# Performance work log

Hardware: AMD Instinct MI355X
Metric: run time of the kernel (lower is better)

Reference implementation:

```python
import jax, jax.numpy as jnp
import numpy as np

B, LQ, LK, E, H, F = 4, 1024, 1024, 1024, 16, 4096
DH = E // H
SCALE = 1.0 / float(np.sqrt(DH))


def _ln(x, g, b, eps=1e-5):
    m = jnp.mean(x, axis=-1, keepdims=True)
    v = jnp.mean((x - m) ** 2, axis=-1, keepdims=True)
    return (x - m) * jax.lax.rsqrt(v + eps) * g + b


def setup_inputs() -> dict:
    key = jax.random.key(0)
    ks = jax.random.split(key, 16)
    s = 0.02
    return {
        "tgt": jax.random.normal(ks[0], (B, LQ, E), jnp.float32),
        "memory": jax.random.normal(ks[1], (B, LK, E), jnp.float32),
        "ln1_g": jnp.ones((E,), jnp.float32),
        "ln1_b": jnp.zeros((E,), jnp.float32),
        "wq": jax.random.normal(ks[2], (E, E), jnp.float32) * s,
        "bq": jnp.zeros((E,), jnp.float32),
        "wk": jax.random.normal(ks[3], (E, E), jnp.float32) * s,
        "bk": jnp.zeros((E,), jnp.float32),
        "wv": jax.random.normal(ks[4], (E, E), jnp.float32) * s,
        "bv": jnp.zeros((E,), jnp.float32),
        "wo": jax.random.normal(ks[5], (E, E), jnp.float32) * s,
        "bo": jnp.zeros((E,), jnp.float32),
        "ln3_g": jnp.ones((E,), jnp.float32),
        "ln3_b": jnp.zeros((E,), jnp.float32),
        "w1": jax.random.normal(ks[6], (E, F), jnp.float32) * s,
        "b1": jnp.zeros((F,), jnp.float32),
        "w2": jax.random.normal(ks[7], (F, E), jnp.float32) * s,
        "b2": jnp.zeros((E,), jnp.float32),
    }


def reference(tgt, memory, ln1_g, ln1_b, wq, bq, wk, bk, wv, bv, wo, bo,
              ln3_g, ln3_b, w1, b1, w2, b2):
    # prenorm cross-attention (dropout=0 / eval mode)
    t2 = _ln(tgt, ln1_g, ln1_b)
    q = (t2 @ wq + bq).reshape(B, LQ, H, DH)
    k = (memory @ wk + bk).reshape(B, LK, H, DH)
    v = (memory @ wv + bv).reshape(B, LK, H, DH)
    scores = jnp.einsum('bqhd,bkhd->bhqk', q, k) * SCALE
    p = jax.nn.softmax(scores, axis=-1)          # [B,H,Lq,Lk]
    attn = jnp.mean(p, axis=1)                   # averaged over heads, like torch need_weights
    o = jnp.einsum('bhqk,bkhd->bqhd', p, v).reshape(B, LQ, E) @ wo + bo
    x = tgt + o
    # prenorm FFN
    t3 = _ln(x, ln3_g, ln3_b)
    ffn = jax.nn.relu(t3 @ w1 + b1) @ w2 + b2
    return x + ffn, attn
```

## Files before the change

kernel.cpp:

```cpp
#include <hip/hip_runtime.h>
#include <hip/hip_bf16.h>

using short8 = __attribute__((ext_vector_type(8))) short;
using f32x4  = __attribute__((ext_vector_type(4))) float;
using u16x4  = __attribute__((ext_vector_type(4))) unsigned short;

#define AS1 __attribute__((address_space(1)))
#define AS3 __attribute__((address_space(3)))

__device__ __forceinline__ unsigned short f2bf(float f) {
    __hip_bfloat16 h = __float2bfloat16(f);
    return __builtin_bit_cast(unsigned short, h);
}

__device__ __forceinline__ float exp2_hw(float x) {
    float r;
    asm("v_exp_f32 %0, %1" : "=v"(r) : "v"(x));
    return r;
}

__device__ __forceinline__ int vperm(int lk) {
    return (lk & ~31) | (((lk >> 2) & 3) * 8) | (((lk >> 4) & 1) * 4) | (lk & 3);
}

__global__ __launch_bounds__(256) void ln_to_bf16(
    const float* __restrict__ X, const float* __restrict__ gw,
    const float* __restrict__ bw, unsigned short* __restrict__ Y)
{
    const int row = blockIdx.x;
    const int tid = threadIdx.x;
    const float4 v = *(const float4*)(X + (size_t)row * 1024 + tid * 4);
    float s  = v.x + v.y + v.z + v.w;
    float s2 = v.x*v.x + v.y*v.y + v.z*v.z + v.w*v.w;
    #pragma unroll
    for (int off = 1; off < 64; off <<= 1) {
        s  += __shfl_xor(s,  off);
        s2 += __shfl_xor(s2, off);
    }
    __shared__ float rs[4], rq[4];
    if ((tid & 63) == 0) { rs[tid >> 6] = s; rq[tid >> 6] = s2; }
    __syncthreads();
    s  = rs[0] + rs[1] + rs[2] + rs[3];
    s2 = rq[0] + rq[1] + rq[2] + rq[3];
    const float mean = s * (1.f / 1024.f);
    const float var  = s2 * (1.f / 1024.f) - mean * mean;
    const float rstd = rsqrtf(var + 1e-5f);
    const float4 gv = *(const float4*)(gw + tid * 4);
    const float4 bv = *(const float4*)(bw + tid * 4);
    u16x4 o;
    o[0] = f2bf((v.x - mean) * rstd * gv.x + bv.x);
    o[1] = f2bf((v.y - mean) * rstd * gv.y + bv.y);
    o[2] = f2bf((v.z - mean) * rstd * gv.z + bv.z);
    o[3] = f2bf((v.w - mean) * rstd * gv.w + bv.w);
    *(u16x4*)(Y + (size_t)row * 1024 + tid * 4) = o;
}

__global__ __launch_bounds__(256) void prep_fused(
    const float* __restrict__ tgt, const float* __restrict__ ln1g,
    const float* __restrict__ ln1b, unsigned short* __restrict__ XA,
    const float* __restrict__ mem, unsigned short* __restrict__ M16,
    const float* __restrict__ wq, const float* __restrict__ wk,
    const float* __restrict__ wv, const float* __restrict__ wo,
    unsigned short* __restrict__ WQT, unsigned short* __restrict__ WKT,
    unsigned short* __restrict__ WVT, unsigned short* __restrict__ WOT,
    const float* __restrict__ w1, unsigned short* __restrict__ W1T,
    const float* __restrict__ w2, unsigned short* __restrict__ W2T)
{
    __shared__ float t[32][33];
    __shared__ float rs[4], rq[4];
    const int bid = blockIdx.x;
    const int tid = threadIdx.x;
    if (bid < 4096) {
        const int row = bid;
        const float4 v = *(const float4*)(tgt + (size_t)row * 1024 + tid * 4);
        float s  = v.x + v.y + v.z + v.w;
        float s2 = v.x*v.x + v.y*v.y + v.z*v.z + v.w*v.w;
        #pragma unroll
        for (int off = 1; off < 64; off <<= 1) {
            s  += __shfl_xor(s,  off);
            s2 += __shfl_xor(s2, off);
        }
        if ((tid & 63) == 0) { rs[tid >> 6] = s; rq[tid >> 6] = s2; }
        __syncthreads();
        s  = rs[0] + rs[1] + rs[2] + rs[3];
        s2 = rq[0] + rq[1] + rq[2] + rq[3];
        const float mean = s * (1.f / 1024.f);
        const float var  = s2 * (1.f / 1024.f) - mean * mean;
        const float rstd = rsqrtf(var + 1e-5f);
        const float4 gv = *(const float4*)(ln1g + tid * 4);
        const float4 bv = *(const float4*)(ln1b + tid * 4);
        u16x4 o;
        o[0] = f2bf((v.x - mean) * rstd * gv.x + bv.x);
        o[1] = f2bf((v.y - mean) * rstd * gv.y + bv.y);
        o[2] = f2bf((v.z - mean) * rstd * gv.z + bv.z);
        o[3] = f2bf((v.w - mean) * rstd * gv.w + bv.w);
        *(u16x4*)(XA + (size_t)row * 1024 + tid * 4) = o;
    } else if (bid < 8192) {
        const int i = (bid - 4096) * 256 + tid;
        float4 v = ((const float4*)mem)[i];
        u16x4 o = { f2bf(v.x), f2bf(v.y), f2bf(v.z), f2bf(v.w) };
        ((u16x4*)M16)[i] = o;
    } else {
        const float* W; unsigned short* Wt; int kb, nb, K;
        if (bid < 12288) {
            const int idx2 = bid - 8192;
            const int which = idx2 >> 10;
            W  = which == 0 ? wq : which == 1 ? wk : which == 2 ? wv : wo;
            Wt = which == 0 ? WQT : which == 1 ? WKT : which == 2 ? WVT : WOT;
            const int idx = idx2 & 1023;
            kb = idx & 31; nb = idx >> 5; K = 1024;
            const int c = tid & 31, r0 = tid >> 5;
            #pragma unroll
            for (int i = 0; i < 4; i++)
                t[r0 + i * 8][c] = W[(size_t)(kb * 32 + r0 + i * 8) * 1024 + nb * 32 + c];
            __syncthreads();
            #pragma unroll
            for (int i = 0; i < 4; i++)
                Wt[(size_t)(nb * 32 + r0 + i * 8) * K + kb * 32 + c] = f2bf(t[c][r0 + i * 8]);
        } else {
            int N;
            if (bid < 16384) { const int idx = bid - 12288; kb = idx % 32;  nb = idx / 32;  K = 1024; N = 4096; W = w1; Wt = W1T; }
            else             { const int idx = bid - 16384; kb = idx % 128; nb = idx / 128; K = 4096; N = 1024; W = w2; Wt = W2T; }
            const int c = tid & 31, r0 = tid >> 5;
            #pragma unroll
            for (int i = 0; i < 4; i++)
                t[r0 + i * 8][c] = W[(size_t)(kb * 32 + r0 + i * 8) * N + nb * 32 + c];
            __syncthreads();
            #pragma unroll
            for (int i = 0; i < 4; i++)
                Wt[(size_t)(nb * 32 + r0 + i * 8) * K + kb * 32 + c] = f2bf(t[c][r0 + i * 8]);
        }
    }
}

template<int EPI, int BN>
__device__ __forceinline__ void gemm_epilogue(
    f32x4 (&acc)[4][BN / 32], int bm, int bn, int wm, int wn, int g, int q16,
    const float* __restrict__ bias, const float* __restrict__ bias2,
    void* __restrict__ outp, void* __restrict__ outp2,
    const float* __restrict__ resid, float oscale, int N)
{
    constexpr int NF = BN / 32;
    const int row0 = bm * 128 + wm * 64;
    const int col0 = bn * BN + wn * (BN / 2);
    const bool isV = (EPI == 4) && (bn * BN >= 1024);
    #pragma unroll
    for (int nf = 0; nf < NF; nf++) {
        const int col = col0 + nf * 16 + q16;
        const float bv = (EPI == 4 && isV) ? bias2[col - 1024] : bias[col];
        #pragma unroll
        for (int mf = 0; mf < 4; mf++) {
            const int rbase = row0 + mf * 16 + g * 4;
            #pragma unroll
            for (int r = 0; r < 4; r++) {
                const int row = rbase + r;
                const float v = acc[mf][nf][r] + bv;
                if constexpr (EPI == 0) {
                    ((unsigned short*)outp)[(size_t)row * N + col] = f2bf(v * oscale);
                } else if constexpr (EPI == 1) {
                    const int bI = row >> 10, lk = row & 1023, hh = col >> 6, dd = col & 63;
                    ((unsigned short*)outp)[((size_t)(bI * 16 + hh) * 64 + dd) * 1024 + vperm(lk)] = f2bf(v);
                } else if constexpr (EPI == 2) {
                    ((unsigned short*)outp)[(size_t)row * N + col] = f2bf(v > 0.f ? v : 0.f);
                } else if constexpr (EPI == 3) {
                    ((float*)outp)[(size_t)row * N + col] = resid[(size_t)row * N + col] + v;
                } else {
                    if (!isV) {
                        ((unsigned short*)outp)[(size_t)row * 1024 + col] = f2bf(v);
                    } else {
                        const int cc = col - 1024;
                        const int bI = row >> 10, lk = row & 1023, hh = cc >> 6, dd = cc & 63;
                        ((unsigned short*)outp2)[((size_t)(bI * 16 + hh) * 64 + dd) * 1024 + vperm(lk)] = f2bf(v);
                    }
                }
            }
        }
    }
}

template<int EPI, int BN, int PF>
__device__ __forceinline__ void gemm_body(
    unsigned short* S,
    const unsigned short* __restrict__ A, const unsigned short* __restrict__ Bt,
    const float* __restrict__ bias, const float* __restrict__ bias2,
    void* __restrict__ outp, void* __restrict__ outp2,
    const float* __restrict__ resid, float oscale, int M, int N, int K,
    int vbid, int vgrid)
{
    constexpr int NF = BN / 32;
    constexpr int LDSH = (128 + BN) * 32;
    const int tid = threadIdx.x;
    const int lane = tid & 63, wave = tid >> 6;
    const int g = lane >> 4, q16 = lane & 15;
    const int wm = wave >> 1, wn = wave & 1;
    const int nb = N / BN;
    const int cpx = vgrid >> 3;
    const int swz = (vbid & 7) * cpx + (vbid >> 3);
    const int bm = swz / nb, bn = swz % nb;

    const unsigned short* aSrc = A  + (size_t)(bm * 128 + (tid >> 2)) * K + (tid & 3) * 8;
    const unsigned short* bSrc = Bt + (size_t)(bn * BN  + (tid >> 2)) * K + (tid & 3) * 8;
    const size_t rowStep = (size_t)64 * K;

    f32x4 acc[4][NF] = {};

    auto STAGE = [&](int slot, int kt) {
        unsigned short* aDst = &S[slot * LDSH] + wave * 512;
        unsigned short* bDst = &S[slot * LDSH + 4096] + wave * 512;
        __builtin_amdgcn_global_load_lds((const AS1 unsigned int*)(aSrc + kt),           (AS3 unsigned int*)aDst,          16, 0, 0);
        __builtin_amdgcn_global_load_lds((const AS1 unsigned int*)(aSrc + rowStep + kt), (AS3 unsigned int*)(aDst + 2048), 16, 0, 0);
        __builtin_amdgcn_global_load_lds((const AS1 unsigned int*)(bSrc + kt),           (AS3 unsigned int*)bDst,          16, 0, 0);
        if constexpr (BN == 128)
            __builtin_amdgcn_global_load_lds((const AS1 unsigned int*)(bSrc + rowStep + kt), (AS3 unsigned int*)(bDst + 2048), 16, 0, 0);
    };
    auto COMPUTE = [&](int slot) {
        const unsigned short* As = &S[slot * LDSH];
        const unsigned short* Bs = As + 4096;
        short8 af[4], bfr[NF];
        #pragma unroll
        for (int i = 0; i < 4; i++)  af[i]  = *(const short8*)(As + (wm * 64 + i * 16 + q16) * 32 + g * 8);
        #pragma unroll
        for (int i = 0; i < NF; i++) bfr[i] = *(const short8*)(Bs + (wn * (BN / 2) + i * 16 + q16) * 32 + g * 8);
        #pragma unroll
        for (int mf = 0; mf < 4; mf++)
            #pragma unroll
            for (int nf = 0; nf < NF; nf++)
                acc[mf][nf] = __builtin_amdgcn_mfma_f32_16x16x32_bf16(af[mf], bfr[nf], acc[mf][nf], 0, 0, 0);
    };

    #pragma unroll
    for (int i = 0; i < PF; i++) STAGE(i, i * 32);
    __syncthreads();
    int p = 0;
    #pragma unroll 1
    for (int kt = PF * 32; kt < K; kt += PF * 32) {
        #pragma unroll
        for (int i = 0; i < PF; i++) STAGE((p ^ 1) * PF + i, kt + i * 32);
        #pragma unroll
        for (int i = 0; i < PF; i++) COMPUTE(p * PF + i);
        __syncthreads();
        p ^= 1;
    }
    #pragma unroll
    for (int i = 0; i < PF; i++) COMPUTE(p * PF + i);

    gemm_epilogue<EPI, BN>(acc, bm, bn, wm, wn, g, q16, bias, bias2,
                           outp, outp2, resid, oscale, N);
}

template<int EPI, int BN, int PF>
__global__ __launch_bounds__(256) void gemm_single(
    const unsigned short* __restrict__ A, const unsigned short* __restrict__ Bt,
    const float* __restrict__ bias, const float* __restrict__ bias2,
    void* __restrict__ outp, void* __restrict__ outp2,
    const float* __restrict__ resid, float oscale, int M, int N, int K)
{
    __shared__ unsigned short S[2 * PF * (128 + BN) * 32];
    gemm_body<EPI, BN, PF>(S, A, Bt, bias, bias2, outp, outp2, resid, oscale,
                           M, N, K, blockIdx.x, gridDim.x);
}

template<int EPI, int BN, int PF>
__global__ __launch_bounds__(256) void gemm_ring3(
    const unsigned short* __restrict__ A, const unsigned short* __restrict__ Bt,
    const float* __restrict__ bias, const float* __restrict__ bias2,
    void* __restrict__ outp, void* __restrict__ outp2,
    const float* __restrict__ resid, float oscale, int M, int N, int K)
{
    constexpr int NF = BN / 32;
    constexpr int LDSH = (128 + BN) * 32;
    constexpr int LPP = PF * (BN == 128 ? 4 : 3);
    __shared__ unsigned short S[3 * PF * LDSH];
    const int tid = threadIdx.x;
    const int lane = tid & 63, wave = tid >> 6;
    const int g = lane >> 4, q16 = lane & 15;
    const int wm = wave >> 1, wn = wave & 1;
    const int nb = N / BN;
    const int cpx = gridDim.x >> 3;
    const int swz = (blockIdx.x & 7) * cpx + (blockIdx.x >> 3);
    const int bm = swz / nb, bn = swz % nb;

    const unsigned short* aSrc = A  + (size_t)(bm * 128 + (tid >> 2)) * K + (tid & 3) * 8;
    const unsigned short* bSrc = Bt + (size_t)(bn * BN  + (tid >> 2)) * K + (tid & 3) * 8;
    const size_t rowStep = (size_t)64 * K;

    f32x4 acc[4][NF] = {};

    auto STAGEPAIR = [&](int pair, int t) {
        #pragma unroll
        for (int i = 0; i < PF; i++) {
            const int kt = t * PF * 32 + i * 32;
            unsigned short* aDst = &S[(pair * PF + i) * LDSH] + wave * 512;
            unsigned short* bDst = &S[(pair * PF + i) * LDSH + 4096] + wave * 512;
            __builtin_amdgcn_global_load_lds((const AS1 unsigned int*)(aSrc + kt),           (AS3 unsigned int*)aDst,          16, 0, 0);
            __builtin_amdgcn_global_load_lds((const AS1 unsigned int*)(aSrc + rowStep + kt), (AS3 unsigned int*)(aDst + 2048), 16, 0, 0);
            __builtin_amdgcn_global_load_lds((const AS1 unsigned int*)(bSrc + kt),           (AS3 unsigned int*)bDst,          16, 0, 0);
            if constexpr (BN == 128)
                __builtin_amdgcn_global_load_lds((const AS1 unsigned int*)(bSrc + rowStep + kt), (AS3 unsigned int*)(bDst + 2048), 16, 0, 0);
        }
    };
    auto COMPUTEPAIR = [&](int pair) {
        #pragma unroll
        for (int s = 0; s < PF; s++) {
            const unsigned short* As = &S[(pair * PF + s) * LDSH];
            const unsigned short* Bs = As + 4096;
            short8 af[4], bfr[NF];
            #pragma unroll
            for (int i = 0; i < 4; i++)  af[i]  = *(const short8*)(As + (wm * 64 + i * 16 + q16) * 32 + g * 8);
            #pragma unroll
            for (int i = 0; i < NF; i++) bfr[i] = *(const short8*)(Bs + (wn * (BN / 2) + i * 16 + q16) * 32 + g * 8);
            #pragma unroll
            for (int mf = 0; mf < 4; mf++)
                #pragma unroll
                for (int nf = 0; nf < NF; nf++)
                    acc[mf][nf] = __builtin_amdgcn_mfma_f32_16x16x32_bf16(af[mf], bfr[nf], acc[mf][nf], 0, 0, 0);
        }
    };

    const int NT = K / (PF * 32);
    STAGEPAIR(0, 0);
    STAGEPAIR(1, 1);
    asm volatile("s_waitcnt vmcnt(%0)" :: "n"(LPP) : "memory");
    __builtin_amdgcn_s_barrier();
    #pragma unroll 1
    for (int t = 0; t < NT; ++t) {
        if (t + 2 < NT) STAGEPAIR((t + 2) % 3, t + 2);
        COMPUTEPAIR(t % 3);
        if (t + 1 < NT) asm volatile("s_waitcnt vmcnt(%0)" :: "n"(LPP) : "memory");
        else            asm volatile("s_waitcnt vmcnt(0)" ::: "memory");
        __builtin_amdgcn_s_barrier();
    }

    gemm_epilogue<EPI, BN>(acc, bm, bn, wm, wn, g, q16, bias, bias2,
                           outp, outp2, resid, oscale, N);
}

__global__ __launch_bounds__(256) void qkv_fused(
    const unsigned short* __restrict__ XA, const unsigned short* __restrict__ WQT,
    const float* __restrict__ bq,
    const unsigned short* __restrict__ M16, const unsigned short* __restrict__ WKT,
    const float* __restrict__ bk, const float* __restrict__ bv,
    unsigned short* __restrict__ Qb, unsigned short* __restrict__ Kb,
    unsigned short* __restrict__ Vt, float qscale)
{
    __shared__ unsigned short S[2 * 2 * 256 * 32];
    if (blockIdx.x < 512)
        gemm_body<0, 64, 2>(S, XA, WQT, bq, nullptr, Qb, nullptr, nullptr,
                            qscale, 4096, 1024, 1024, blockIdx.x, 512);
    else
        gemm_body<4, 128, 2>(S, M16, WKT, bk, bv, Kb, Vt, nullptr,
                             1.0f, 4096, 2048, 1024, blockIdx.x - 512, 512);
}

__global__ __launch_bounds__(256) void att_pv(
    const unsigned short* __restrict__ Q, const unsigned short* __restrict__ Kb,
    const unsigned short* __restrict__ Vt, unsigned short* __restrict__ O,
    float* __restrict__ LINV)
{
    __shared__ unsigned short Ks[2][2048];
    __shared__ unsigned short Vs[2][2048];
    const int tid = threadIdx.x, lane = tid & 63, wave = tid >> 6;
    const int g = lane >> 4, q16 = lane & 15;
    const int bh = blockIdx.x & 63;
    const int qt = blockIdx.x >> 6;
    const int b = bh >> 4, h = bh & 15;
    const int qbase = qt * 128 + wave * 32;

    const int rowK = wave * 8 + (lane >> 3);
    const int cK   = (lane & 7) ^ (rowK & 7);
    const int rowV = wave * 16 + (lane >> 2);
    const int cV   = (lane & 3) ^ (rowV & 3);
    const unsigned short* kSrc = Kb + ((size_t)(b * 1024 + rowK)) * 1024 + h * 64 + cK * 8;
    const unsigned short* vSrc = Vt + ((size_t)(bh * 64 + rowV)) * 1024 + cV * 8;

    short8 qf[2][2];
    #pragma unroll
    for (int nf = 0; nf < 2; nf++)
        #pragma unroll
        for (int ds = 0; ds < 2; ds++)
            qf[nf][ds] = *(const short8*)(Q + (size_t)(b * 1024 + qbase + nf * 16 + q16) * 1024 + h * 64 + ds * 32 + g * 8);

    f32x4 oacc[4][2] = {};
    float lsum[2] = {0.f, 0.f};

    auto STAGE = [&](int buf, int kc) {
        __builtin_amdgcn_global_load_lds((const AS1 unsigned int*)(kSrc + (size_t)kc * 1024),
                                         (AS3 unsigned int*)(&Ks[buf][0] + wave * 512), 16, 0, 0);
        __builtin_amdgcn_global_load_lds((const AS1 unsigned int*)(vSrc + kc),
                                         (AS3 unsigned int*)(&Vs[buf][0] + wave * 512), 16, 0, 0);
    };
    auto BODY = [&](int buf) {
        short8 kf[2][2], vf[4];
        #pragma unroll
        for (int kt = 0; kt < 2; kt++)
            #pragma unroll
            for (int ds = 0; ds < 2; ds++)
                kf[kt][ds] = *(const short8*)(&Ks[buf][0] + (kt * 16 + q16) * 64 + ((ds * 4 + g) ^ (q16 & 7)) * 8);
        #pragma unroll
        for (int mf = 0; mf < 4; mf++)
            vf[mf] = *(const short8*)(&Vs[buf][0] + (mf * 16 + q16) * 32 + (g ^ (q16 & 3)) * 8);
        f32x4 sacc[2][2] = {};
        #pragma unroll
        for (int kt = 0; kt < 2; kt++)
            #pragma unroll
            for (int nf = 0; nf < 2; nf++) {
                sacc[kt][nf] = __builtin_amdgcn_mfma_f32_16x16x32_bf16(kf[kt][0], qf[nf][0], sacc[kt][nf], 0, 0, 0);
                sacc[kt][nf] = __builtin_amdgcn_mfma_f32_16x16x32_bf16(kf[kt][1], qf[nf][1], sacc[kt][nf], 0, 0, 0);
            }
        float ps[2][2][4];
        #pragma unroll
        for (int kt = 0; kt < 2; kt++)
            #pragma unroll
            for (int nf = 0; nf < 2; nf++)
                #pragma unroll
                for (int r = 0; r < 4; r++)
                    ps[kt][nf][r] = exp2_hw(sacc[kt][nf][r]);
        #pragma unroll
        for (int nf = 0; nf < 2; nf++)
            lsum[nf] += ps[0][nf][0] + ps[0][nf][1] + ps[0][nf][2] + ps[0][nf][3]
                      + ps[1][nf][0] + ps[1][nf][1] + ps[1][nf][2] + ps[1][nf][3];
        short8 pbf[2];
        #pragma unroll
        for (int nf = 0; nf < 2; nf++) {
            pbf[nf][0] = (short)f2bf(ps[0][nf][0]);
            pbf[nf][1] = (short)f2bf(ps[0][nf][1]);
            pbf[nf][2] = (short)f2bf(ps[0][nf][2]);
            pbf[nf][3] = (short)f2bf(ps[0][nf][3]);
            pbf[nf][4] = (short)f2bf(ps[1][nf][0]);
            pbf[nf][5] = (short)f2bf(ps[1][nf][1]);
            pbf[nf][6] = (short)f2bf(ps[1][nf][2]);
            pbf[nf][7] = (short)f2bf(ps[1][nf][3]);
        }
        #pragma unroll
        for (int mf = 0; mf < 4; mf++)
            #pragma unroll
            for (int nf = 0; nf < 2; nf++)
                oacc[mf][nf] = __builtin_amdgcn_mfma_f32_16x16x32_bf16(vf[mf], pbf[nf], oacc[mf][nf], 0, 0, 0);
    };

    STAGE(0, 0);
    __syncthreads();
    int buf = 0;
    #pragma unroll 1
    for (int kc = 0; kc < 1024; kc += 32) {
        if (kc + 32 < 1024) STAGE(buf ^ 1, kc + 32);
        BODY(buf);
        __syncthreads();
        buf ^= 1;
    }
    #pragma unroll
    for (int nf = 0; nf < 2; nf++) {
        lsum[nf] += __shfl_xor(lsum[nf], 16);
        lsum[nf] += __shfl_xor(lsum[nf], 32);
    }

    #pragma unroll
    for (int nf = 0; nf < 2; nf++) {
        const float inv = 1.0f / lsum[nf];
        if (g == 0) LINV[(size_t)bh * 1024 + qbase + nf * 16 + q16] = inv;
        #pragma unroll
        for (int mf = 0; mf < 4; mf++) {
            u16x4 o;
            #pragma unroll
            for (int r = 0; r < 4; r++) o[r] = f2bf(oacc[mf][nf][r] * inv);
            *(u16x4*)(O + (size_t)(b * 1024 + qbase + nf * 16 + q16) * 1024 + h * 64 + mf * 16 + g * 4) = o;
        }
    }
}

__global__ __launch_bounds__(256) void att_mean(
    const unsigned short* __restrict__ Q, const unsigned short* __restrict__ Kb,
    const float* __restrict__ LINV, float* __restrict__ out1)
{
    __shared__ unsigned short Qs[2][2048];
    const int tid = threadIdx.x;
    const int lane = tid & 63, wave = tid >> 6;
    const int g = lane >> 4, q16 = lane & 15;
    const int kb = blockIdx.x & 7;
    const int qb = (blockIdx.x >> 3) & 31;
    const int b = blockIdx.x >> 8;
    const int qbase = qb * 32;
    const int kbase = kb * 128 + wave * 32;

    const int rowQ = wave * 8 + (lane >> 3);
    const int cQ   = (lane & 7) ^ (rowQ & 7);
    const unsigned short* qSrc = Q + (size_t)(b * 1024 + qbase + rowQ) * 1024 + cQ * 8;

    f32x4 facc[2][2] = {};

    auto STAGE = [&](int buf, int h) {
        __builtin_amdgcn_global_load_lds((const AS1 unsigned int*)(qSrc + h * 64),
                                         (AS3 unsigned int*)(&Qs[buf][0] + wave * 512), 16, 0, 0);
    };
    auto LOADK = [&](short8 (&kf)[2][2], f32x4 (&li)[2], int h) {
        #pragma unroll
        for (int nf = 0; nf < 2; nf++)
            #pragma unroll
            for (int ds = 0; ds < 2; ds++)
                kf[nf][ds] = *(const short8*)(Kb + (size_t)(b * 1024 + kbase + nf * 16 + q16) * 1024 + h * 64 + ds * 32 + g * 8);
        const float* lp = LINV + (size_t)(b * 16 + h) * 1024 + qbase;
        #pragma unroll
        for (int mf = 0; mf < 2; mf++)
            li[mf] = *(const f32x4*)(lp + mf * 16 + g * 4);
    };
    auto COMP = [&](int buf, short8 (&kf)[2][2], f32x4 (&li)[2]) {
        short8 qfr[2][2];
        #pragma unroll
        for (int mf = 0; mf < 2; mf++)
            #pragma unroll
            for (int ds = 0; ds < 2; ds++)
                qfr[mf][ds] = *(const short8*)(&Qs[buf][0] + (mf * 16 + q16) * 64 + ((ds * 4 + g) ^ (q16 & 7)) * 8);
        #pragma unroll
        for (int nf = 0; nf < 2; nf++) {
            f32x4 sacc[2] = {};
            #pragma unroll
            for (int mf = 0; mf < 2; mf++) {
                sacc[mf] = __builtin_amdgcn_mfma_f32_16x16x32_bf16(qfr[mf][0], kf[nf][0], sacc[mf], 0, 0, 0);
                sacc[mf] = __builtin_amdgcn_mfma_f32_16x16x32_bf16(qfr[mf][1], kf[nf][1], sacc[mf], 0, 0, 0);
            }
            #pragma unroll
            for (int mf = 0; mf < 2; mf++)
                #pragma unroll
                for (int r = 0; r < 4; r++)
                    facc[mf][nf][r] = fmaf(exp2_hw(sacc[mf][r]), li[mf][r], facc[mf][nf][r]);
        }
    };

    short8 kA[2][2], kB[2][2];
    f32x4 liA[2], liB[2];
    STAGE(0, 0); LOADK(kA, liA, 0);
    __syncthreads();
    #pragma unroll 1
    for (int h = 0; h < 16; h += 2) {
        STAGE(1, h + 1); LOADK(kB, liB, h + 1);
        COMP(0, kA, liA);
        __syncthreads();
        if (h + 2 < 16) { STAGE(0, h + 2); LOADK(kA, liA, h + 2); }
        COMP(1, kB, liB);
        __syncthreads();
    }

    #pragma unroll
    for (int mf = 0; mf < 2; mf++)
        #pragma unroll
        for (int nf = 0; nf < 2; nf++)
            #pragma unroll
            for (int r = 0; r < 4; r++)
                out1[(size_t)(b * 1024 + qbase + mf * 16 + g * 4 + r) * 1024 + kbase + nf * 16 + q16]
                    = facc[mf][nf][r] * 0.0625f;
}

extern "C" void kernel_launch(void* const* d_in, const int* in_sizes, int n_in,
                              void* d_out, int out_size, void* d_ws, size_t ws_size,
                              hipStream_t stream)
{
    (void)in_sizes; (void)n_in; (void)out_size; (void)ws_size;
    const float* tgt  = (const float*)d_in[0];
    const float* mem  = (const float*)d_in[1];
    const float* ln1g = (const float*)d_in[2];
    const float* ln1b = (const float*)d_in[3];
    const float* wq   = (const float*)d_in[4];
    const float* bq   = (const float*)d_in[5];
    const float* wk   = (const float*)d_in[6];
    const float* bk   = (const float*)d_in[7];
    const float* wv   = (const float*)d_in[8];
    const float* bv   = (const float*)d_in[9];
    const float* wo   = (const float*)d_in[10];
    const float* bo   = (const float*)d_in[11];
    const float* ln3g = (const float*)d_in[12];
    const float* ln3b = (const float*)d_in[13];
    const float* w1   = (const float*)d_in[14];
    const float* b1   = (const float*)d_in[15];
    const float* w2   = (const float*)d_in[16];
    const float* b2   = (const float*)d_in[17];

    char* ws = (char*)d_ws;
    unsigned short* XA  = (unsigned short*)(ws);
    unsigned short* M16 = (unsigned short*)(ws + ((size_t)8  << 20));
    unsigned short* WQT = (unsigned short*)(ws + ((size_t)16 << 20));
    unsigned short* WKT = (unsigned short*)(ws + ((size_t)18 << 20));
    unsigned short* WVT = (unsigned short*)(ws + ((size_t)20 << 20));
    unsigned short* WOT = (unsigned short*)(ws + ((size_t)22 << 20));
    unsigned short* W1T = (unsigned short*)(ws + ((size_t)24 << 20));
    unsigned short* W2T = (unsigned short*)(ws + ((size_t)32 << 20));
    unsigned short* Qb  = (unsigned short*)(ws + ((size_t)40 << 20));
    unsigned short* Kb  = (unsigned short*)(ws + ((size_t)48 << 20));
    unsigned short* Vt  = (unsigned short*)(ws + ((size_t)56 << 20));
    unsigned short* O16 = (unsigned short*)(ws + ((size_t)64 << 20));
    unsigned short* H16 = (unsigned short*)(ws + ((size_t)72 << 20));
    float*          LNV = (float*)(ws + ((size_t)104 << 20));
    float* xout = (float*)d_out;
    float* attn = xout + (size_t)4 * 1024 * 1024;

    const float QSCALE = 0.125f * 1.4426950408889634f;

    prep_fused<<<20480, 256, 0, stream>>>(tgt, ln1g, ln1b, XA, mem, M16,
                                          wq, wk, wv, wo, WQT, WKT, WVT, WOT,
                                          w1, W1T, w2, W2T);

    qkv_fused<<<1024, 256, 0, stream>>>(XA, WQT, bq, M16, WKT, bk, bv, Qb, Kb, Vt, QSCALE);

    att_pv<<<512, 256, 0, stream>>>(Qb, Kb, Vt, O16, LNV);
    att_mean<<<1024, 256, 0, stream>>>(Qb, Kb, LNV, attn);

    gemm_single<3, 64, 2><<<32 * 16, 256, 0, stream>>>(O16, WOT, bo, nullptr, xout, nullptr, tgt, 1.0f, 4096, 1024, 1024);
    ln_to_bf16<<<4096, 256, 0, stream>>>(xout, ln3g, ln3b, XA);
    gemm_single<2, 128, 2><<<32 * 32, 256, 0, stream>>>(XA, W1T, b1, nullptr, H16, nullptr, nullptr, 1.0f, 4096, 4096, 1024);
    gemm_ring3<3, 64, 2><<<32 * 16, 256, 0, stream>>>(H16, W2T, b2, nullptr, xout, nullptr, xout, 1.0f, 4096, 1024, 4096);
}
```

Measured before the change: 261.3 us.

## Fuse head-mean attention weights and output projection into one launch

Merges the independent att_mean kernel and the Wo projection GEMM into a single launch with 1536 blocks. The first 512 blocks run the GEMM body and the rest compute the head-averaged attention weights, sharing one LDS buffer. This removes one kernel launch and lets the two workloads overlap on the GPU. The cost is that the shared LDS allocation is sized for the GEMM, which may reduce occupancy for the att_mean blocks.

```diff
diff --git a/kernel.cpp b/kernel.cpp
--- a/kernel.cpp
+++ b/kernel.cpp
@@ -468,17 +468,17 @@
     }
 }
 
-__global__ __launch_bounds__(256) void att_mean(
+__device__ __forceinline__ void att_mean_body(
+    unsigned short* Qs,
     const unsigned short* __restrict__ Q, const unsigned short* __restrict__ Kb,
-    const float* __restrict__ LINV, float* __restrict__ out1)
-{
-    __shared__ unsigned short Qs[2][2048];
+    const float* __restrict__ LINV, float* __restrict__ out1, int vbid)
+{
     const int tid = threadIdx.x;
     const int lane = tid & 63, wave = tid >> 6;
     const int g = lane >> 4, q16 = lane & 15;
-    const int kb = blockIdx.x & 7;
-    const int qb = (blockIdx.x >> 3) & 31;
-    const int b = blockIdx.x >> 8;
+    const int kb = vbid & 7;
+    const int qb = (vbid >> 3) & 31;
+    const int b = vbid >> 8;
     const int qbase = qb * 32;
     const int kbase = kb * 128 + wave * 32;
 
@@ -490,7 +490,7 @@
 
     auto STAGE = [&](int buf, int h) {
         __builtin_amdgcn_global_load_lds((const AS1 unsigned int*)(qSrc + h * 64),
-                                         (AS3 unsigned int*)(&Qs[buf][0] + wave * 512), 16, 0, 0);
+                                         (AS3 unsigned int*)(Qs + buf * 2048 + wave * 512), 16, 0, 0);
     };
     auto LOADK = [&](short8 (&kf)[2][2], f32x4 (&li)[2], int h) {
         #pragma unroll
@@ -509,7 +509,7 @@
         for (int mf = 0; mf < 2; mf++)
             #pragma unroll
             for (int ds = 0; ds < 2; ds++)
-                qfr[mf][ds] = *(const short8*)(&Qs[buf][0] + (mf * 16 + q16) * 64 + ((ds * 4 + g) ^ (q16 & 7)) * 8);
+                qfr[mf][ds] = *(const short8*)(Qs + buf * 2048 + (mf * 16 + q16) * 64 + ((ds * 4 + g) ^ (q16 & 7)) * 8);
         #pragma unroll
         for (int nf = 0; nf < 2; nf++) {
             f32x4 sacc[2] = {};
@@ -548,6 +548,20 @@
             for (int r = 0; r < 4; r++)
                 out1[(size_t)(b * 1024 + qbase + mf * 16 + g * 4 + r) * 1024 + kbase + nf * 16 + q16]
                     = facc[mf][nf][r] * 0.0625f;
+}
+
+__global__ __launch_bounds__(256) void wo_attmean_fused(
+    const unsigned short* __restrict__ O16, const unsigned short* __restrict__ WOT,
+    const float* __restrict__ bo, float* __restrict__ xout, const float* __restrict__ tgt,
+    const unsigned short* __restrict__ Qb, const unsigned short* __restrict__ Kb,
+    const float* __restrict__ LNV, float* __restrict__ attn)
+{
+    __shared__ unsigned short S[2 * 2 * (128 + 64) * 32];
+    if (blockIdx.x < 512)
+        gemm_body<3, 64, 2>(S, O16, WOT, bo, nullptr, xout, nullptr, tgt,
+                            1.0f, 4096, 1024, 1024, blockIdx.x, 512);
+    else
+        att_mean_body(S, Qb, Kb, LNV, attn, blockIdx.x - 512);
 }
 
 extern "C" void kernel_launch(void* const* d_in, const int* in_sizes, int n_in,
@@ -601,9 +615,10 @@
     qkv_fused<<<1024, 256, 0, stream>>>(XA, WQT, bq, M16, WKT, bk, bv, Qb, Kb, Vt, QSCALE);
 
     att_pv<<<512, 256, 0, stream>>>(Qb, Kb, Vt, O16, LNV);
-    att_mean<<<1024, 256, 0, stream>>>(Qb, Kb, LNV, attn);
-
-    gemm_single<3, 64, 2><<<32 * 16, 256, 0, stream>>>(O16, WOT, bo, nullptr, xout, nullptr, tgt, 1.0f, 4096, 1024, 1024);
+
+    wo_attmean_fused<<<1536, 256, 0, stream>>>(O16, WOT, bo, xout, tgt,
+                                               Qb, Kb, LNV, attn);
+
     ln_to_bf16<<<4096, 256, 0, stream>>>(xout, ln3g, ln3b, XA);
     gemm_single<2, 128, 2><<<32 * 32, 256, 0, stream>>>(XA, W1T, b1, nullptr, H16, nullptr, nullptr, 1.0f, 4096, 4096, 1024);
     gemm_ring3<3, 64, 2><<<32 * 16, 256, 0, stream>>>(H16, W2T, b2, nullptr, xout, nullptr, xout, 1.0f, 4096, 1024, 4096);
```

New measurement: 257.3 us (median of 3 runs). About the same (-1.5%).
